# Optimization experiments

Measured on AMD Instinct MI355X. Metric: run time of the kernel, lower is better.

Reference implementation:

```python
import jax, jax.numpy as jnp
import numpy as np

D_MODEL = 512; D_STATE = 64; D_CONV = 4; HEADDIM = 64
D_INNER = 2 * D_MODEL              # expand=2
NHEADS = D_INNER // HEADDIM        # 16
CONV_DIM = D_INNER + 2 * D_STATE   # 1152
D_IN_PROJ = 2 * D_INNER + 2 * D_STATE + NHEADS  # 2192
BATCH, SEQ = 4, 1024
EPS = 1e-5


def rmsnorm(x, w):
    return x * jax.lax.rsqrt(jnp.mean(x * x, axis=-1, keepdims=True) + EPS) * w


def mamba2(u, in_w, conv_w, conv_b, dt_bias, A_log, D, gnorm_w, out_w):
    b, l, _ = u.shape
    zxbcdt = u @ in_w.T                                  # [b,l,D_IN_PROJ]
    z = zxbcdt[..., :D_INNER]
    xBC = zxbcdt[..., D_INNER:D_INNER + CONV_DIM]
    dt = jax.nn.softplus(zxbcdt[..., -NHEADS:] + dt_bias)  # [b,l,h]
    # causal depthwise conv1d (kernel D_CONV, left pad) + silu
    pad = jnp.pad(xBC, ((0, 0), (D_CONV - 1, 0), (0, 0)))
    acc = conv_b
    for k in range(D_CONV):
        acc = acc + pad[:, k:k + l, :] * conv_w[:, k]
    xBC = jax.nn.silu(acc)
    x = xBC[..., :D_INNER].reshape(b, l, NHEADS, HEADDIM)
    Bm = xBC[..., D_INNER:D_INNER + D_STATE]             # [b,l,n]
    Cm = xBC[..., D_INNER + D_STATE:]                    # [b,l,n]
    A = -jnp.exp(A_log)                                  # [h]
    decay = jnp.exp(dt * A)                              # [b,l,h]
    dtx = dt[..., None] * x                              # [b,l,h,p]

    def step(h, inp):
        dec, dx, Bt, Ct = inp
        h = h * dec[:, :, None, None] + dx[..., None] * Bt[:, None, None, :]
        y = jnp.einsum('bhpn,bn->bhp', h, Ct)
        return h, y

    h0 = jnp.zeros((b, NHEADS, HEADDIM, D_STATE), u.dtype)
    _, ys = jax.lax.scan(step, h0, (decay.transpose(1, 0, 2),
                                    dtx.transpose(1, 0, 2, 3),
                                    Bm.transpose(1, 0, 2),
                                    Cm.transpose(1, 0, 2)))
    y = ys.transpose(1, 0, 2, 3) + x * D[None, None, :, None]  # [b,l,h,p]
    y = y.reshape(b, l, D_INNER)
    y = rmsnorm(y * jax.nn.silu(z), gnorm_w)             # gated RMSNorm
    return y @ out_w.T


def setup_inputs() -> dict:
    key = jax.random.key(0)
    ks = iter(jax.random.split(key, 32))
    def rn(shape, scale=0.02):
        return jax.random.normal(next(ks), shape, dtype=jnp.float32) * scale
    inp = {
        'x': jax.random.normal(next(ks), (BATCH, SEQ, D_MODEL), dtype=jnp.float32),
        'norm_w': jnp.ones((D_MODEL,), jnp.float32),
    }
    for p in ('f', 'b'):
        inp[p + '_in_w'] = rn((D_IN_PROJ, D_MODEL))
        inp[p + '_conv_w'] = rn((CONV_DIM, D_CONV), 0.1)
        inp[p + '_conv_b'] = jnp.zeros((CONV_DIM,), jnp.float32)
        inp[p + '_dt_bias'] = rn((NHEADS,), 0.5)
        inp[p + '_A_log'] = jnp.log(jnp.arange(1, NHEADS + 1, dtype=jnp.float32))
        inp[p + '_D'] = jnp.ones((NHEADS,), jnp.float32)
        inp[p + '_gnorm_w'] = jnp.ones((D_INNER,), jnp.float32)
        inp[p + '_out_w'] = rn((D_MODEL, D_INNER))
    inp['proj_w'] = rn((D_MODEL, 2 * D_MODEL))
    return inp


def reference(x, norm_w,
              f_in_w, f_conv_w, f_conv_b, f_dt_bias, f_A_log, f_D, f_gnorm_w, f_out_w,
              b_in_w, b_conv_w, b_conv_b, b_dt_bias, b_A_log, b_D, b_gnorm_w, b_out_w,
              proj_w):
    h = rmsnorm(x, norm_w)
    fo = mamba2(h, f_in_w, f_conv_w, f_conv_b, f_dt_bias, f_A_log, f_D, f_gnorm_w, f_out_w)
    bo = jnp.flip(mamba2(jnp.flip(h, 1), b_in_w, b_conv_w, b_conv_b, b_dt_bias,
                         b_A_log, b_D, b_gnorm_w, b_out_w), 1)
    return x + jnp.concatenate([fo, bo], axis=-1) @ proj_w.T
```

## Files before the change

### kernel.cpp

```cpp
#include <hip/hip_runtime.h>
#include <math.h>

typedef unsigned short u16;
typedef __bf16  bf16x8 __attribute__((ext_vector_type(8)));
typedef float   f32x4  __attribute__((ext_vector_type(4)));
typedef unsigned short u16x8 __attribute__((ext_vector_type(8)));

#define SEQ 1024
#define MR  4096
#define DIP 2192
#define DI  1024
#define NH  16
#define CD  1152
#define NCH 32
#define CT  32
#define NIN (DIP*512)
#define NOUT (512*1024)

__device__ __forceinline__ u16 f2bf(float f) {
  union { float f; unsigned u; } v; v.f = f;
  unsigned r = v.u + 0x7FFFu + ((v.u >> 16) & 1u);
  return (u16)(r >> 16);
}
__device__ __forceinline__ float bf2f(u16 h) {
  union { unsigned u; float f; } v; v.u = ((unsigned)h) << 16; return v.f;
}
__device__ __forceinline__ void splitbf(float v, u16& h, u16& l) {
  h = f2bf(v); l = f2bf(v - bf2f(h));
}
__device__ __forceinline__ float sigm(float x){ return 1.f/(1.f+__expf(-x)); }

__device__ __forceinline__ unsigned packbf(float v) {
  u16 hh, ll; splitbf(v, hh, ll);
  return (unsigned)hh | ((unsigned)ll << 16);
}
__device__ __forceinline__ float unpackf(unsigned w) {
  return bf2f((u16)w) + bf2f((u16)(w >> 16));
}

__device__ __forceinline__ void split8(const float* p, bf16x8& H, bf16x8& L) {
  float4 a = *(const float4*)p, b = *(const float4*)(p+4);
  u16x8 hu, lu; u16 hh, ll;
  splitbf(a.x,hh,ll); hu[0]=hh; lu[0]=ll;
  splitbf(a.y,hh,ll); hu[1]=hh; lu[1]=ll;
  splitbf(a.z,hh,ll); hu[2]=hh; lu[2]=ll;
  splitbf(a.w,hh,ll); hu[3]=hh; lu[3]=ll;
  splitbf(b.x,hh,ll); hu[4]=hh; lu[4]=ll;
  splitbf(b.y,hh,ll); hu[5]=hh; lu[5]=ll;
  splitbf(b.z,hh,ll); hu[6]=hh; lu[6]=ll;
  splitbf(b.w,hh,ll); hu[7]=hh; lu[7]=ll;
  H = __builtin_bit_cast(bf16x8, hu);
  L = __builtin_bit_cast(bf16x8, lu);
}
__device__ __forceinline__ void unpack8(const unsigned* p, bf16x8& H, bf16x8& L) {
  uint4 a = *(const uint4*)p, b = *(const uint4*)(p+4);
  u16x8 hu, lu;
  hu[0]=(u16)a.x; lu[0]=(u16)(a.x>>16);
  hu[1]=(u16)a.y; lu[1]=(u16)(a.y>>16);
  hu[2]=(u16)a.z; lu[2]=(u16)(a.z>>16);
  hu[3]=(u16)a.w; lu[3]=(u16)(a.w>>16);
  hu[4]=(u16)b.x; lu[4]=(u16)(b.x>>16);
  hu[5]=(u16)b.y; lu[5]=(u16)(b.y>>16);
  hu[6]=(u16)b.z; lu[6]=(u16)(b.z>>16);
  hu[7]=(u16)b.w; lu[7]=(u16)(b.w>>16);
  H = __builtin_bit_cast(bf16x8, hu);
  L = __builtin_bit_cast(bf16x8, lu);
}
__device__ __forceinline__ void unpack8s(const unsigned* p, int stride, bf16x8& H, bf16x8& L) {
  u16x8 hu, lu;
  #pragma unroll
  for (int jj=0;jj<8;jj++){ unsigned w = p[(size_t)jj*stride]; hu[jj]=(u16)w; lu[jj]=(u16)(w>>16); }
  H = __builtin_bit_cast(bf16x8, hu);
  L = __builtin_bit_cast(bf16x8, lu);
}

__device__ __forceinline__ void gl16(const u16* g, u16* l) {
  __builtin_amdgcn_global_load_lds((const __attribute__((address_space(1))) void*)g,
                                   (__attribute__((address_space(3))) void*)l,
                                   16, 0, 0);
}

__global__ __launch_bounds__(256) void cast_all(
  const float* __restrict__ f_in, const float* __restrict__ b_in,
  const float* __restrict__ f_out, const float* __restrict__ b_out,
  const float* __restrict__ proj,
  u16* __restrict__ H, u16* __restrict__ L)
{
  int i = blockIdx.x*256 + threadIdx.x;
  constexpr int TOT = 2*NIN + 3*NOUT;
  if (i >= TOT) return;
  float v;
  if (i < NIN)               v = f_in[i];
  else if (i < 2*NIN)        v = b_in[i-NIN];
  else if (i < 2*NIN+NOUT)   v = f_out[i-2*NIN];
  else if (i < 2*NIN+2*NOUT) v = b_out[i-2*NIN-NOUT];
  else                       v = proj[i-2*NIN-2*NOUT];
  u16 hh, ll; splitbf(v, hh, ll);
  H[i] = hh; L[i] = ll;
}

__global__ __launch_bounds__(256) void rmsnorm_x(const float* __restrict__ x,
                                                 const float* __restrict__ w,
                                                 u16* __restrict__ hbh,
                                                 u16* __restrict__ hbl){
  int m = blockIdx.x, tid = threadIdx.x;
  const float* xr = x + (size_t)m*512;
  float2 v = *(const float2*)&xr[tid*2];
  float ss = v.x*v.x + v.y*v.y;
  #pragma unroll
  for (int off=32; off; off>>=1) ss += __shfl_xor(ss, off, 64);
  __shared__ float red[4];
  if ((tid&63)==0) red[tid>>6] = ss;
  __syncthreads();
  float total = red[0]+red[1]+red[2]+red[3];
  float rs = rsqrtf(total*(1.f/512.f) + 1e-5f);
  float2 w2 = *(const float2*)&w[tid*2];
  u16 h0,l0,h1,l1;
  splitbf(v.x*rs*w2.x, h0, l0);
  splitbf(v.y*rs*w2.y, h1, l1);
  *(unsigned*)&hbh[(size_t)m*512 + tid*2] = (unsigned)h0 | ((unsigned)h1<<16);
  *(unsigned*)&hbl[(size_t)m*512 + tid*2] = (unsigned)l0 | ((unsigned)l1<<16);
}

__global__ __launch_bounds__(256) void gemm_in(
    const u16* __restrict__ Ah, const u16* __restrict__ Al,
    const u16* __restrict__ Wh, const u16* __restrict__ Wl,
    float* __restrict__ C0)
{
  constexpr int K = 512;
  constexpr int N = DIP;
  __shared__ __align__(16) u16 sAh[128*32];
  __shared__ __align__(16) u16 sAl[128*32];
  __shared__ __align__(16) u16 sBh[128*32];
  __shared__ __align__(16) u16 sBl[128*32];
  const int tid = threadIdx.x;
  const int dir = blockIdx.z;
  const int m0 = blockIdx.x * 128;
  const int n0 = blockIdx.y * 128;
  const int lane = tid & 63;
  const int wid  = tid >> 6;
  const u16* wh_p = Wh + (size_t)dir*NIN;
  const u16* wl_p = Wl + (size_t)dir*NIN;
  const int j0 = wid, j1 = wid + 4;
  const int cp = lane & 3;
  auto goff = [&](int j, bool isB)->size_t {
    int row = 16*j + (lane>>2);
    int s = (row>>1) & 3;
    int kc = (cp ^ s) * 8;
    int grow;
    if (!isB) {
      grow = m0 + row;
      if (dir) grow = (grow & ~1023) + (1023 - (grow & 1023));
    } else {
      grow = n0 + row;
      if (grow >= N) grow = N-1;
    }
    return (size_t)grow*K + kc;
  };
  const size_t a0 = goff(j0,false), a1 = goff(j1,false);
  const size_t b0 = goff(j0,true),  b1 = goff(j1,true);
  const int wm = (wid & 1) * 64;
  const int wn = (wid >> 1) * 64;
  const int quad = lane >> 4;
  const int l16  = lane & 15;
  const int qx = quad ^ ((l16>>1)&3);
  const int baseA = ((wm + l16)*4 + qx)*8;
  const int baseB = ((wn + l16)*4 + qx)*8;
  f32x4 acc[4][4] = {};
  for (int kt = 0; kt < K; kt += 32) {
    __syncthreads();
    gl16(Ah + a0 + kt, &sAh[j0*512]);  gl16(Ah + a1 + kt, &sAh[j1*512]);
    gl16(Al + a0 + kt, &sAl[j0*512]);  gl16(Al + a1 + kt, &sAl[j1*512]);
    gl16(wh_p + b0 + kt, &sBh[j0*512]);  gl16(wh_p + b1 + kt, &sBh[j1*512]);
    gl16(wl_p + b0 + kt, &sBl[j0*512]);  gl16(wl_p + b1 + kt, &sBl[j1*512]);
    __syncthreads();
    bf16x8 ah[4], al[4], bh[4], bl[4];
    #pragma unroll
    for (int i=0;i<4;i++) {
      ah[i] = *(const bf16x8*)&sAh[baseA + i*512];
      al[i] = *(const bf16x8*)&sAl[baseA + i*512];
    }
    #pragma unroll
    for (int j=0;j<4;j++) {
      bh[j] = *(const bf16x8*)&sBh[baseB + j*512];
      bl[j] = *(const bf16x8*)&sBl[baseB + j*512];
    }
    #pragma unroll
    for (int i=0;i<4;i++)
      #pragma unroll
      for (int j=0;j<4;j++) {
        f32x4 t = __builtin_amdgcn_mfma_f32_16x16x32_bf16(ah[i], bl[j], acc[i][j], 0,0,0);
        t       = __builtin_amdgcn_mfma_f32_16x16x32_bf16(al[i], bh[j], t,         0,0,0);
        acc[i][j] = __builtin_amdgcn_mfma_f32_16x16x32_bf16(ah[i], bh[j], t,       0,0,0);
      }
  }
  #pragma unroll
  for (int i=0;i<4;i++)
  #pragma unroll
  for (int j=0;j<4;j++)
  #pragma unroll
  for (int r=0;r<4;r++) {
    int mo = m0 + wm + i*16 + quad*4 + r;
    int no = n0 + wn + j*16 + l16;
    if (no < N) C0[((size_t)dir*MR + mo)*DIP + no] = acc[i][j][r];
  }
}

template<int MODE>
__global__ __launch_bounds__(256) void gemm_out(
    const u16* __restrict__ Ah, const u16* __restrict__ Al,
    const u16* __restrict__ Wh, const u16* __restrict__ Wl,
    float* __restrict__ C0, const float* __restrict__ X0,
    u16* __restrict__ C1h, u16* __restrict__ C1l)
{
  constexpr int K = 1024;
  __shared__ __align__(16) u16 sAh[64*32];
  __shared__ __align__(16) u16 sAl[64*32];
  __shared__ __align__(16) u16 sBh[128*32];
  __shared__ __align__(16) u16 sBl[128*32];
  const int tid = threadIdx.x;
  const int dir = blockIdx.z;
  const int m0 = blockIdx.x * 64;
  const int n0 = blockIdx.y * 128;
  const int lane = tid & 63;
  const int wid  = tid >> 6;
  const u16* ah_p = Ah + ((MODE==1) ? (size_t)dir*MR*K : 0);
  const u16* al_p = Al + ((MODE==1) ? (size_t)dir*MR*K : 0);
  const u16* wh_p = Wh + ((MODE==1) ? (size_t)dir*NOUT : 0);
  const u16* wl_p = Wl + ((MODE==1) ? (size_t)dir*NOUT : 0);
  const int cp = lane & 3;
  auto goff = [&](int j, bool isB)->size_t {
    int row = 16*j + (lane>>2);
    int s = (row>>1) & 3;
    int kc = (cp ^ s) * 8;
    int grow = (isB ? n0 : m0) + row;
    return (size_t)grow*K + kc;
  };
  const size_t a0 = goff(wid,false);
  const size_t b0 = goff(wid,true), b1 = goff(wid+4,true);
  const int quad = lane >> 4;
  const int l16  = lane & 15;
  const int qx = quad ^ ((l16>>1)&3);
  const int baseA = (l16*4 + qx)*8;
  const int baseB = ((wid*32 + l16)*4 + qx)*8;
  f32x4 acc[4][2] = {};
  for (int kt = 0; kt < K; kt += 32) {
    __syncthreads();
    gl16(ah_p + a0 + kt, &sAh[wid*512]);
    gl16(al_p + a0 + kt, &sAl[wid*512]);
    gl16(wh_p + b0 + kt, &sBh[wid*512]);  gl16(wh_p + b1 + kt, &sBh[(wid+4)*512]);
    gl16(wl_p + b0 + kt, &sBl[wid*512]);  gl16(wl_p + b1 + kt, &sBl[(wid+4)*512]);
    __syncthreads();
    bf16x8 ah[4], al[4], bh[2], bl[2];
    #pragma unroll
    for (int i=0;i<4;i++) {
      ah[i] = *(const bf16x8*)&sAh[baseA + i*512];
      al[i] = *(const bf16x8*)&sAl[baseA + i*512];
    }
    #pragma unroll
    for (int j=0;j<2;j++) {
      bh[j] = *(const bf16x8*)&sBh[baseB + j*512];
      bl[j] = *(const bf16x8*)&sBl[baseB + j*512];
    }
    #pragma unroll
    for (int i=0;i<4;i++)
      #pragma unroll
      for (int j=0;j<2;j++) {
        f32x4 t = __builtin_amdgcn_mfma_f32_16x16x32_bf16(ah[i], bl[j], acc[i][j], 0,0,0);
        t       = __builtin_amdgcn_mfma_f32_16x16x32_bf16(al[i], bh[j], t,         0,0,0);
        acc[i][j] = __builtin_amdgcn_mfma_f32_16x16x32_bf16(ah[i], bh[j], t,       0,0,0);
      }
  }
  #pragma unroll
  for (int i=0;i<4;i++)
  #pragma unroll
  for (int j=0;j<2;j++)
  #pragma unroll
  for (int r=0;r<4;r++) {
    int mo = m0 + i*16 + quad*4 + r;
    int no = n0 + wid*32 + j*16 + l16;
    float v = acc[i][j][r];
    if (MODE==1) {
      int ro = mo;
      if (dir) ro = (mo & ~1023) + (1023 - (mo & 1023));
      u16 hh, ll; splitbf(v, hh, ll);
      C1h[(size_t)ro*DI + dir*512 + no] = hh;
      C1l[(size_t)ro*DI + dir*512 + no] = ll;
    } else {
      C0[(size_t)mo*512 + no] = v + X0[(size_t)mo*512 + no];
    }
  }
}

__global__ __launch_bounds__(320) void conv_dt(
  const float* __restrict__ Z,
  const float* __restrict__ f_cw, const float* __restrict__ f_cb,
  const float* __restrict__ b_cw, const float* __restrict__ b_cb,
  const float* __restrict__ f_dtb, const float* __restrict__ b_dtb,
  unsigned* __restrict__ xconv,
  unsigned* __restrict__ Bc, unsigned* __restrict__ Cc,
  float* __restrict__ dtq)
{
  int bm = blockIdx.x;
  int dir = bm >> 12;
  int t = bm & 1023;
  const float* cw  = dir ? b_cw : f_cw;
  const float* cb  = dir ? b_cb : f_cb;
  const float* dtb = dir ? b_dtb : f_dtb;
  int tid = threadIdx.x;
  if (tid < 288) {
    int c0 = tid*4;
    const float* zbase = Z + (size_t)(bm-3)*DIP + 1024 + c0;
    float4 w0 = *(const float4*)&cw[c0*4];
    float4 w1 = *(const float4*)&cw[(c0+1)*4];
    float4 w2 = *(const float4*)&cw[(c0+2)*4];
    float4 w3 = *(const float4*)&cw[(c0+3)*4];
    float4 z0 = {0,0,0,0}, z1 = {0,0,0,0}, z2 = {0,0,0,0};
    float4 z3 = *(const float4*)(zbase + 3*(size_t)DIP);
    if (t >= 3) {
      z0 = *(const float4*)(zbase);
      z1 = *(const float4*)(zbase + (size_t)DIP);
      z2 = *(const float4*)(zbase + 2*(size_t)DIP);
    } else {
      if (t >= 1) z2 = *(const float4*)(zbase + 2*(size_t)DIP);
      if (t >= 2) z1 = *(const float4*)(zbase + (size_t)DIP);
    }
    float4 a = *(const float4*)&cb[c0];
    a.x += z0.x*w0.x + z1.x*w0.y + z2.x*w0.z + z3.x*w0.w;
    a.y += z0.y*w1.x + z1.y*w1.y + z2.y*w1.z + z3.y*w1.w;
    a.z += z0.z*w2.x + z1.z*w2.y + z2.z*w2.z + z3.z*w2.w;
    a.w += z0.w*w3.x + z1.w*w3.y + z2.w*w3.z + z3.w*w3.w;
    float4 v;
    v.x = a.x * sigm(a.x); v.y = a.y * sigm(a.y);
    v.z = a.z * sigm(a.z); v.w = a.w * sigm(a.w);
    uint4 pv;
    pv.x = packbf(v.x); pv.y = packbf(v.y);
    pv.z = packbf(v.z); pv.w = packbf(v.w);
    if (c0 < 1024)      *(uint4*)&xconv[(size_t)bm*DI + c0] = pv;
    else if (c0 < 1088) *(uint4*)&Bc[(size_t)bm*64 + (c0-1024)] = pv;
    else                *(uint4*)&Cc[(size_t)bm*64 + (c0-1088)] = pv;
  }
  if (tid < NH) {
    float dtraw = Z[(size_t)bm*DIP + 2176 + tid] + dtb[tid];
    float dt = (dtraw > 20.f) ? dtraw : log1pf(__expf(dtraw));
    dtq[(size_t)bm*NH + tid] = dt;
  }
}

__global__ __launch_bounds__(256) void scan_mfma(
  const float* __restrict__ dtq, const unsigned* __restrict__ xconv,
  const unsigned* __restrict__ Bc, const unsigned* __restrict__ Cc,
  const float* __restrict__ f_Al, const float* __restrict__ b_Al,
  float* __restrict__ yraw, float* __restrict__ cumdec, float* __restrict__ S)
{
  __shared__ __align__(16) u16 sMh[4][32*40];
  __shared__ __align__(16) u16 sMl[4][32*40];
  __shared__ float scum[4][32];
  __shared__ float sdt[4][32];
  int bx = blockIdx.x;
  int hq = bx & 3, chunk = (bx>>2)&(NCH-1), dirb = bx>>7;
  int w = threadIdx.x >> 6, lane = threadIdx.x & 63;
  int h = hq*4 + w;
  int base_row = dirb*1024 + chunk*CT;
  const int quad = lane >> 4, l16 = lane & 15;
  const float* Al = (dirb >= 4) ? b_Al : f_Al;
  float A = -__expf(Al[h]);
  float dtl = 0.f, cum = 0.f;
  if (lane < 32) { dtl = dtq[(size_t)(base_row + lane)*16 + h]; cum = dtl; }
  #pragma unroll
  for (int off=1; off<32; off<<=1) {
    int src = (lane >= off) ? lane-off : lane;
    float o = __shfl(cum, src);
    if (lane >= off && lane < 32) cum += o;
  }
  if (lane < 32) {
    sdt[w][lane]  = dtl;
    scum[w][lane] = cum;
    cumdec[(size_t)(base_row + lane)*16 + h] = __expf(A*cum);
  }
  bf16x8 chf[2][2], clf[2][2], bhf[2][2], blf[2][2];
  #pragma unroll
  for (int i=0;i<2;i++)
  #pragma unroll
  for (int kk=0;kk<2;kk++) {
    unpack8(Cc + (size_t)(base_row + 16*i + l16)*64 + kk*32 + quad*8, chf[i][kk], clf[i][kk]);
    unpack8(Bc + (size_t)(base_row + 16*i + l16)*64 + kk*32 + quad*8, bhf[i][kk], blf[i][kk]);
  }
  f32x4 g[2][2];
  __builtin_amdgcn_s_setprio(1);
  #pragma unroll
  for (int i=0;i<2;i++)
  #pragma unroll
  for (int j=0;j<2;j++) {
    f32x4 acc = {};
    #pragma unroll
    for (int kk=0;kk<2;kk++) {
      acc = __builtin_amdgcn_mfma_f32_16x16x32_bf16(chf[i][kk], blf[j][kk], acc, 0,0,0);
      acc = __builtin_amdgcn_mfma_f32_16x16x32_bf16(clf[i][kk], bhf[j][kk], acc, 0,0,0);
      acc = __builtin_amdgcn_mfma_f32_16x16x32_bf16(chf[i][kk], bhf[j][kk], acc, 0,0,0);
    }
    g[i][j] = acc;
  }
  __builtin_amdgcn_s_setprio(0);
  float ctt[2][4];
  #pragma unroll
  for (int i=0;i<2;i++)
  #pragma unroll
  for (int r=0;r<4;r++) ctt[i][r] = scum[w][16*i + quad*4 + r];
  #pragma unroll
  for (int j=0;j<2;j++) {
    int s = 16*j + l16;
    float cts = scum[w][s];
    float dts = sdt[w][s];
    #pragma unroll
    for (int i=0;i<2;i++)
    #pragma unroll
    for (int r=0;r<4;r++) {
      int t = 16*i + quad*4 + r;
      float mv = (s <= t) ? g[i][j][r] * __expf(A*(ctt[i][r]-cts)) * dts : 0.f;
      u16 hh, ll; splitbf(mv, hh, ll);
      sMh[w][t*40 + s] = hh;
      sMl[w][t*40 + s] = ll;
    }
  }
  bf16x8 xhf[4], xlf[4];
  const unsigned* xp = xconv + (size_t)(base_row + quad*8)*1024 + h*64 + l16;
  #pragma unroll
  for (int jp=0;jp<4;jp++) unpack8s(xp + 16*jp, 1024, xhf[jp], xlf[jp]);
  bf16x8 mhf[2], mlf[2];
  #pragma unroll
  for (int i=0;i<2;i++) {
    mhf[i] = *(const bf16x8*)&sMh[w][(16*i + l16)*40 + quad*8];
    mlf[i] = *(const bf16x8*)&sMl[w][(16*i + l16)*40 + quad*8];
  }
  __builtin_amdgcn_s_setprio(1);
  #pragma unroll
  for (int i=0;i<2;i++)
  #pragma unroll
  for (int jp=0;jp<4;jp++) {
    f32x4 acc = {};
    acc = __builtin_amdgcn_mfma_f32_16x16x32_bf16(mhf[i], xlf[jp], acc, 0,0,0);
    acc = __builtin_amdgcn_mfma_f32_16x16x32_bf16(mlf[i], xhf[jp], acc, 0,0,0);
    acc = __builtin_amdgcn_mfma_f32_16x16x32_bf16(mhf[i], xhf[jp], acc, 0,0,0);
    #pragma unroll
    for (int r=0;r<4;r++)
      yraw[(size_t)(base_row + 16*i + quad*4 + r)*1024 + h*64 + 16*jp + l16] = acc[r];
  }
  __builtin_amdgcn_s_setprio(0);
  float wv[8];
  float ct31 = scum[w][31];
  #pragma unroll
  for (int jj=0;jj<8;jj++) {
    int s = quad*8 + jj;
    wv[jj] = sdt[w][s] * __expf(A*(ct31 - scum[w][s]));
  }
  bf16x8 wbh[4], wbl[4];
  #pragma unroll
  for (int j2=0;j2<4;j2++) {
    u16x8 hu, lu; u16 hh, ll;
    #pragma unroll
    for (int jj=0;jj<8;jj++) {
      float b = unpackf(Bc[(size_t)(base_row + quad*8 + jj)*64 + 16*j2 + l16]);
      splitbf(wv[jj]*b, hh, ll); hu[jj]=hh; lu[jj]=ll;
    }
    wbh[j2] = __builtin_bit_cast(bf16x8, hu);
    wbl[j2] = __builtin_bit_cast(bf16x8, lu);
  }
  size_t inst = ((size_t)(dirb*16+h)*NCH + chunk)*4096;
  __builtin_amdgcn_s_setprio(1);
  #pragma unroll
  for (int mp=0;mp<4;mp++)
  #pragma unroll
  for (int j2=0;j2<4;j2++) {
    f32x4 acc = {};
    acc = __builtin_amdgcn_mfma_f32_16x16x32_bf16(xhf[mp], wbl[j2], acc, 0,0,0);
    acc = __builtin_amdgcn_mfma_f32_16x16x32_bf16(xlf[mp], wbh[j2], acc, 0,0,0);
    acc = __builtin_amdgcn_mfma_f32_16x16x32_bf16(xhf[mp], wbh[j2], acc, 0,0,0);
    #pragma unroll
    for (int r=0;r<4;r++)
      S[inst + (size_t)(16*mp + quad*4 + r)*64 + 16*j2 + l16] = acc[r];
  }
  __builtin_amdgcn_s_setprio(0);
}

__global__ __launch_bounds__(256) void scan_comb(
  const float* __restrict__ cumdec, float* __restrict__ S)
{
  int ih = blockIdx.x >> 4;
  int sub = blockIdx.x & 15;
  int dirb = ih >> 4, h = ih & 15;
  int elem = sub*256 + threadIdx.x;
  size_t base = (size_t)ih*NCH*4096 + elem;
  float hr = 0.f;
  for (int c=0;c<NCH;c++) {
    float P = cumdec[((size_t)(dirb*1024 + c*CT + CT-1))*16 + h];
    float s = S[base + c*4096];
    S[base + c*4096] = __builtin_bit_cast(float, packbf(hr));
    hr = fmaf(hr, P, s);
  }
}

__global__ __launch_bounds__(256) void scan_y2(
  const unsigned* __restrict__ Cc, const float* __restrict__ cumdec,
  const float* __restrict__ S, float* __restrict__ yraw)
{
  int bx = blockIdx.x;
  int hq = bx & 3, chunk = (bx>>2)&(NCH-1), dirb = bx>>7;
  if (chunk == 0) return;
  int w = threadIdx.x >> 6, lane = threadIdx.x & 63;
  int h = hq*4 + w;
  int row0 = dirb*1024 + chunk*CT;
  const int quad = lane>>4, l16 = lane&15;
  size_t inst = ((size_t)(dirb*16+h)*NCH + chunk)*4096;
  float at[2][4];
  #pragma unroll
  for (int i=0;i<2;i++)
  #pragma unroll
  for (int r=0;r<4;r++)
    at[i][r] = cumdec[(size_t)(row0 + 16*i + quad*4 + r)*16 + h];
  bf16x8 chf[2][2], clf[2][2];
  #pragma unroll
  for (int i=0;i<2;i++)
  #pragma unroll
  for (int kk=0;kk<2;kk++)
    unpack8(Cc + (size_t)(row0 + 16*i + l16)*64 + kk*32 + quad*8, chf[i][kk], clf[i][kk]);
  const unsigned* Sp = (const unsigned*)S;
  bf16x8 hhf[4][2], hlf[4][2];
  #pragma unroll
  for (int j=0;j<4;j++)
  #pragma unroll
  for (int kk=0;kk<2;kk++)
    unpack8(Sp + inst + (size_t)(16*j + l16)*64 + kk*32 + quad*8, hhf[j][kk], hlf[j][kk]);
  __builtin_amdgcn_s_setprio(1);
  #pragma unroll
  for (int i=0;i<2;i++)
  #pragma unroll
  for (int j=0;j<4;j++) {
    f32x4 acc = {};
    #pragma unroll
    for (int kk=0;kk<2;kk++) {
      acc = __builtin_amdgcn_mfma_f32_16x16x32_bf16(chf[i][kk], hlf[j][kk], acc, 0,0,0);
      acc = __builtin_amdgcn_mfma_f32_16x16x32_bf16(clf[i][kk], hhf[j][kk], acc, 0,0,0);
      acc = __builtin_amdgcn_mfma_f32_16x16x32_bf16(chf[i][kk], hhf[j][kk], acc, 0,0,0);
    }
    #pragma unroll
    for (int r=0;r<4;r++) {
      size_t idx = (size_t)(row0 + 16*i + quad*4 + r)*1024 + h*64 + 16*j + l16;
      yraw[idx] += at[i][r]*acc[r];
    }
  }
  __builtin_amdgcn_s_setprio(0);
}

__global__ __launch_bounds__(256) void gate_norm(
  const float* __restrict__ yraw, const unsigned* __restrict__ xconv,
  const float* __restrict__ Z,
  const float* __restrict__ f_D, const float* __restrict__ b_D,
  const float* __restrict__ f_gw, const float* __restrict__ b_gw,
  u16* __restrict__ ygh, u16* __restrict__ ygl)
{
  int bm = blockIdx.x, tid = threadIdx.x;
  int dir = bm >> 12;
  const float* Dp = dir ? b_D : f_D;
  const float* gw = dir ? b_gw : f_gw;
  int c0 = tid*4;
  float4 y4 = *(const float4*)&yraw [(size_t)bm*DI + c0];
  uint4  xw = *(const uint4*)&xconv[(size_t)bm*DI + c0];
  float4 z4 = *(const float4*)&Z[(size_t)bm*DIP + c0];
  float Dv = Dp[c0>>6];
  float4 x4;
  x4.x = unpackf(xw.x); x4.y = unpackf(xw.y);
  x4.z = unpackf(xw.z); x4.w = unpackf(xw.w);
  float4 v;
  v.x = (y4.x + x4.x*Dv) * (z4.x * sigm(z4.x));
  v.y = (y4.y + x4.y*Dv) * (z4.y * sigm(z4.y));
  v.z = (y4.z + x4.z*Dv) * (z4.z * sigm(z4.z));
  v.w = (y4.w + x4.w*Dv) * (z4.w * sigm(z4.w));
  float ss = v.x*v.x + v.y*v.y + v.z*v.z + v.w*v.w;
  #pragma unroll
  for (int off=32; off; off>>=1) ss += __shfl_xor(ss, off, 64);
  __shared__ float red[4];
  if ((tid&63)==0) red[tid>>6] = ss;
  __syncthreads();
  float total = red[0]+red[1]+red[2]+red[3];
  float rs = rsqrtf(total*(1.f/1024.f) + 1e-5f);
  float4 g4 = *(const float4*)&gw[c0];
  ushort4 hh, ll;
  splitbf(v.x*rs*g4.x, hh.x, ll.x);
  splitbf(v.y*rs*g4.y, hh.y, ll.y);
  splitbf(v.z*rs*g4.z, hh.z, ll.z);
  splitbf(v.w*rs*g4.w, hh.w, ll.w);
  *(ushort4*)&ygh[(size_t)bm*DI + c0] = hh;
  *(ushort4*)&ygl[(size_t)bm*DI + c0] = ll;
}

extern "C" void kernel_launch(void* const* d_in, const int* in_sizes, int n_in,
                              void* d_out, int out_size, void* d_ws, size_t ws_size,
                              hipStream_t stream)
{
  const float* x        = (const float*)d_in[0];
  const float* norm_w   = (const float*)d_in[1];
  const float* f_in_w   = (const float*)d_in[2];
  const float* f_conv_w = (const float*)d_in[3];
  const float* f_conv_b = (const float*)d_in[4];
  const float* f_dt_bias= (const float*)d_in[5];
  const float* f_A_log  = (const float*)d_in[6];
  const float* f_D      = (const float*)d_in[7];
  const float* f_gw     = (const float*)d_in[8];
  const float* f_out_w  = (const float*)d_in[9];
  const float* b_in_w   = (const float*)d_in[10];
  const float* b_conv_w = (const float*)d_in[11];
  const float* b_conv_b = (const float*)d_in[12];
  const float* b_dt_bias= (const float*)d_in[13];
  const float* b_A_log  = (const float*)d_in[14];
  const float* b_D      = (const float*)d_in[15];
  const float* b_gw     = (const float*)d_in[16];
  const float* b_out_w  = (const float*)d_in[17];
  const float* proj_w   = (const float*)d_in[18];

  char* ws = (char*)d_ws;
  size_t off = 0;
  auto alloc = [&](size_t bytes)->char* {
    char* p = ws + off; off = (off + bytes + 255) & ~(size_t)255; return p;
  };
  constexpr size_t WTOT = 2*(size_t)NIN + 3*(size_t)NOUT;
  u16*   hbh   = (u16*)  alloc((size_t)MR*512*2);
  u16*   hbl   = (u16*)  alloc((size_t)MR*512*2);
  u16*   wH    = (u16*)  alloc(WTOT*2);
  u16*   wL    = (u16*)  alloc(WTOT*2);
  float* Z     = (float*)alloc(2*(size_t)MR*DIP*4);
  unsigned* xconv = (unsigned*)alloc(2*(size_t)MR*DI*4);
  unsigned* Bc    = (unsigned*)alloc(2*(size_t)MR*64*4);
  unsigned* Cc    = (unsigned*)alloc(2*(size_t)MR*64*4);
  float* dtq   = (float*)alloc(2*(size_t)MR*NH*4);
  float* cumdec= (float*)alloc(2*(size_t)MR*NH*4);
  float* S     = (float*)alloc((size_t)4096*4096*4);
  float* yraw  = (float*)alloc(2*(size_t)MR*DI*4);
  u16* wih = wH;                   u16* wil = wL;
  u16* woh = wH + 2*(size_t)NIN;   u16* wol = wL + 2*(size_t)NIN;
  u16* wph = woh + 2*(size_t)NOUT; u16* wpl = wol + 2*(size_t)NOUT;
  u16* ycath = (u16*)((char*)S);
  u16* ycatl = (u16*)((char*)S + ((size_t)MR*DI*2));
  u16* ygh   = (u16*)((char*)S + 2*((size_t)MR*DI*2));
  u16* ygl   = (u16*)((char*)S + 4*((size_t)MR*DI*2));

  cast_all<<<(int)((WTOT+255)/256),256,0,stream>>>(f_in_w, b_in_w, f_out_w, b_out_w, proj_w, wH, wL);

  rmsnorm_x<<<MR,256,0,stream>>>(x, norm_w, hbh, hbl);
  gemm_in<<<dim3(32,18,2),256,0,stream>>>(hbh, hbl, wih, wil, Z);
  conv_dt<<<2*MR,320,0,stream>>>(Z, f_conv_w, f_conv_b, b_conv_w, b_conv_b,
                                 f_dt_bias, b_dt_bias, xconv, Bc, Cc, dtq);
  scan_mfma<<<1024,256,0,stream>>>(dtq, xconv, Bc, Cc, f_A_log, b_A_log,
                                   yraw, cumdec, S);
  scan_comb<<<2048,256,0,stream>>>(cumdec, S);
  scan_y2<<<1024,256,0,stream>>>(Cc, cumdec, S, yraw);
  gate_norm<<<2*MR,256,0,stream>>>(yraw, xconv, Z, f_D, b_D, f_gw, b_gw, ygh, ygl);
  gemm_out<1><<<dim3(64,4,2),256,0,stream>>>(ygh, ygl, woh, wol, nullptr, nullptr, ycath, ycatl);
  gemm_out<2><<<dim3(64,4,1),256,0,stream>>>(ycath, ycatl, wph, wpl, (float*)d_out, x, nullptr, nullptr);
}
```

Baseline: 376.9 us.

## Fuse chunk-state output scan with gated RMSNorm and write into Z buffer

Merges the inter-chunk y correction kernel and the gated RMSNorm kernel into one 1024-thread kernel. Each block covers one 32-row chunk across all 16 heads and stages the gated values in a large LDS tile to compute the row RMS. This removes the read-modify-write of yraw between kernels and one launch. The normalized bf16 hi/lo output is written into the no-longer-needed xBC columns of Z, and the out-projection GEMM reads it there with a strided row pitch. In exchange it uses about 130KB of LDS per block, which limits occupancy to one block per CU and leaves only 256 blocks in the grid.

```diff
diff --git a/kernel.cpp b/kernel.cpp
--- a/kernel.cpp
+++ b/kernel.cpp
@@ -16,6 +16,7 @@
 #define CT  32
 #define NIN (DIP*512)
 #define NOUT (512*1024)
+#define ZROW 4384
 
 __device__ __forceinline__ u16 f2bf(float f) {
   union { float f; unsigned u; } v; v.f = f;
@@ -38,20 +39,6 @@
   return bf2f((u16)w) + bf2f((u16)(w >> 16));
 }
 
-__device__ __forceinline__ void split8(const float* p, bf16x8& H, bf16x8& L) {
-  float4 a = *(const float4*)p, b = *(const float4*)(p+4);
-  u16x8 hu, lu; u16 hh, ll;
-  splitbf(a.x,hh,ll); hu[0]=hh; lu[0]=ll;
-  splitbf(a.y,hh,ll); hu[1]=hh; lu[1]=ll;
-  splitbf(a.z,hh,ll); hu[2]=hh; lu[2]=ll;
-  splitbf(a.w,hh,ll); hu[3]=hh; lu[3]=ll;
-  splitbf(b.x,hh,ll); hu[4]=hh; lu[4]=ll;
-  splitbf(b.y,hh,ll); hu[5]=hh; lu[5]=ll;
-  splitbf(b.z,hh,ll); hu[6]=hh; lu[6]=ll;
-  splitbf(b.w,hh,ll); hu[7]=hh; lu[7]=ll;
-  H = __builtin_bit_cast(bf16x8, hu);
-  L = __builtin_bit_cast(bf16x8, lu);
-}
 __device__ __forceinline__ void unpack8(const unsigned* p, bf16x8& H, bf16x8& L) {
   uint4 a = *(const uint4*)p, b = *(const uint4*)(p+4);
   u16x8 hu, lu;
@@ -214,6 +201,7 @@
     u16* __restrict__ C1h, u16* __restrict__ C1l)
 {
   constexpr int K = 1024;
+  constexpr int AS = (MODE==1) ? ZROW : 1024;
   __shared__ __align__(16) u16 sAh[64*32];
   __shared__ __align__(16) u16 sAl[64*32];
   __shared__ __align__(16) u16 sBh[128*32];
@@ -224,8 +212,8 @@
   const int n0 = blockIdx.y * 128;
   const int lane = tid & 63;
   const int wid  = tid >> 6;
-  const u16* ah_p = Ah + ((MODE==1) ? (size_t)dir*MR*K : 0);
-  const u16* al_p = Al + ((MODE==1) ? (size_t)dir*MR*K : 0);
+  const u16* ah_p = Ah + ((MODE==1) ? (size_t)dir*MR*AS : 0);
+  const u16* al_p = Al + ((MODE==1) ? (size_t)dir*MR*AS : 0);
   const u16* wh_p = Wh + ((MODE==1) ? (size_t)dir*NOUT : 0);
   const u16* wl_p = Wl + ((MODE==1) ? (size_t)dir*NOUT : 0);
   const int cp = lane & 3;
@@ -234,7 +222,7 @@
     int s = (row>>1) & 3;
     int kc = (cp ^ s) * 8;
     int grow = (isB ? n0 : m0) + row;
-    return (size_t)grow*K + kc;
+    return (size_t)grow*(isB ? (size_t)K : (size_t)AS) + kc;
   };
   const size_t a0 = goff(wid,false);
   const size_t b0 = goff(wid,true), b1 = goff(wid+4,true);
@@ -500,98 +488,118 @@
   }
 }
 
-__global__ __launch_bounds__(256) void scan_y2(
+__global__ __launch_bounds__(1024) void scan_y2_gate(
   const unsigned* __restrict__ Cc, const float* __restrict__ cumdec,
-  const float* __restrict__ S, float* __restrict__ yraw)
-{
+  const float* __restrict__ S, const float* __restrict__ yraw,
+  const unsigned* __restrict__ xconv, const float* Z, u16* zt,
+  const float* __restrict__ f_D, const float* __restrict__ b_D,
+  const float* __restrict__ f_gw, const float* __restrict__ b_gw)
+{
+  __shared__ float vbuf[32][1028];
+  __shared__ float red[32][17];
+  __shared__ float rsb[32];
   int bx = blockIdx.x;
-  int hq = bx & 3, chunk = (bx>>2)&(NCH-1), dirb = bx>>7;
-  if (chunk == 0) return;
+  int chunk = bx & (NCH-1), dirb = bx >> 5;
   int w = threadIdx.x >> 6, lane = threadIdx.x & 63;
-  int h = hq*4 + w;
+  int h = w;
+  int dir = dirb >> 2;
   int row0 = dirb*1024 + chunk*CT;
   const int quad = lane>>4, l16 = lane&15;
-  size_t inst = ((size_t)(dirb*16+h)*NCH + chunk)*4096;
-  float at[2][4];
+  const float* Dp  = dir ? b_D  : f_D;
+  const float* gwp = dir ? b_gw : f_gw;
+  float Dv = Dp[h];
+
+  f32x4 acc[2][4] = {};
+  float at[2][4] = {};
+  if (chunk > 0) {
+    size_t inst = ((size_t)(dirb*16+h)*NCH + chunk)*4096;
+    #pragma unroll
+    for (int i=0;i<2;i++)
+    #pragma unroll
+    for (int r=0;r<4;r++)
+      at[i][r] = cumdec[(size_t)(row0 + 16*i + quad*4 + r)*16 + h];
+    bf16x8 chf[2][2], clf[2][2];
+    #pragma unroll
+    for (int i=0;i<2;i++)
+    #pragma unroll
+    for (int kk=0;kk<2;kk++)
+      unpack8(Cc + (size_t)(row0 + 16*i + l16)*64 + kk*32 + quad*8, chf[i][kk], clf[i][kk]);
+    const unsigned* Sp = (const unsigned*)S;
+    __builtin_amdgcn_s_setprio(1);
+    #pragma unroll
+    for (int j=0;j<4;j++) {
+      bf16x8 hhf[2], hlf[2];
+      #pragma unroll
+      for (int kk=0;kk<2;kk++)
+        unpack8(Sp + inst + (size_t)(16*j + l16)*64 + kk*32 + quad*8, hhf[kk], hlf[kk]);
+      #pragma unroll
+      for (int i=0;i<2;i++) {
+        f32x4 a2 = acc[i][j];
+        #pragma unroll
+        for (int kk=0;kk<2;kk++) {
+          a2 = __builtin_amdgcn_mfma_f32_16x16x32_bf16(chf[i][kk], hlf[kk], a2, 0,0,0);
+          a2 = __builtin_amdgcn_mfma_f32_16x16x32_bf16(clf[i][kk], hhf[kk], a2, 0,0,0);
+          a2 = __builtin_amdgcn_mfma_f32_16x16x32_bf16(chf[i][kk], hhf[kk], a2, 0,0,0);
+        }
+        acc[i][j] = a2;
+      }
+    }
+    __builtin_amdgcn_s_setprio(0);
+  }
+  float pss[2][4] = {};
   #pragma unroll
   for (int i=0;i<2;i++)
   #pragma unroll
-  for (int r=0;r<4;r++)
-    at[i][r] = cumdec[(size_t)(row0 + 16*i + quad*4 + r)*16 + h];
-  bf16x8 chf[2][2], clf[2][2];
+  for (int r=0;r<4;r++) {
+    int t = 16*i + quad*4 + r;
+    size_t g = (size_t)(row0 + t);
+    #pragma unroll
+    for (int j=0;j<4;j++) {
+      int c = h*64 + 16*j + l16;
+      float yv = yraw[g*1024 + c];
+      float xv = unpackf(xconv[g*1024 + c]);
+      float zv = Z[g*DIP + c];
+      float v = (yv + xv*Dv + at[i][r]*acc[i][j][r]) * (zv * sigm(zv));
+      vbuf[t][c] = v;
+      pss[i][r] += v*v;
+    }
+  }
   #pragma unroll
   for (int i=0;i<2;i++)
   #pragma unroll
-  for (int kk=0;kk<2;kk++)
-    unpack8(Cc + (size_t)(row0 + 16*i + l16)*64 + kk*32 + quad*8, chf[i][kk], clf[i][kk]);
-  const unsigned* Sp = (const unsigned*)S;
-  bf16x8 hhf[4][2], hlf[4][2];
-  #pragma unroll
-  for (int j=0;j<4;j++)
-  #pragma unroll
-  for (int kk=0;kk<2;kk++)
-    unpack8(Sp + inst + (size_t)(16*j + l16)*64 + kk*32 + quad*8, hhf[j][kk], hlf[j][kk]);
-  __builtin_amdgcn_s_setprio(1);
+  for (int r=0;r<4;r++) {
+    float s2 = pss[i][r];
+    s2 += __shfl_xor(s2, 1, 64);
+    s2 += __shfl_xor(s2, 2, 64);
+    s2 += __shfl_xor(s2, 4, 64);
+    s2 += __shfl_xor(s2, 8, 64);
+    if (l16 == 0) red[16*i + quad*4 + r][w] = s2;
+  }
+  __syncthreads();
+  if (threadIdx.x < 32) {
+    int t = threadIdx.x;
+    float tot = 0.f;
+    #pragma unroll
+    for (int ww=0; ww<16; ww++) tot += red[t][ww];
+    rsb[t] = rsqrtf(tot*(1.f/1024.f) + 1e-5f);
+  }
+  __syncthreads();
   #pragma unroll
   for (int i=0;i<2;i++)
   #pragma unroll
-  for (int j=0;j<4;j++) {
-    f32x4 acc = {};
-    #pragma unroll
-    for (int kk=0;kk<2;kk++) {
-      acc = __builtin_amdgcn_mfma_f32_16x16x32_bf16(chf[i][kk], hlf[j][kk], acc, 0,0,0);
-      acc = __builtin_amdgcn_mfma_f32_16x16x32_bf16(clf[i][kk], hhf[j][kk], acc, 0,0,0);
-      acc = __builtin_amdgcn_mfma_f32_16x16x32_bf16(chf[i][kk], hhf[j][kk], acc, 0,0,0);
-    }
-    #pragma unroll
-    for (int r=0;r<4;r++) {
-      size_t idx = (size_t)(row0 + 16*i + quad*4 + r)*1024 + h*64 + 16*j + l16;
-      yraw[idx] += at[i][r]*acc[r];
-    }
-  }
-  __builtin_amdgcn_s_setprio(0);
-}
-
-__global__ __launch_bounds__(256) void gate_norm(
-  const float* __restrict__ yraw, const unsigned* __restrict__ xconv,
-  const float* __restrict__ Z,
-  const float* __restrict__ f_D, const float* __restrict__ b_D,
-  const float* __restrict__ f_gw, const float* __restrict__ b_gw,
-  u16* __restrict__ ygh, u16* __restrict__ ygl)
-{
-  int bm = blockIdx.x, tid = threadIdx.x;
-  int dir = bm >> 12;
-  const float* Dp = dir ? b_D : f_D;
-  const float* gw = dir ? b_gw : f_gw;
-  int c0 = tid*4;
-  float4 y4 = *(const float4*)&yraw [(size_t)bm*DI + c0];
-  uint4  xw = *(const uint4*)&xconv[(size_t)bm*DI + c0];
-  float4 z4 = *(const float4*)&Z[(size_t)bm*DIP + c0];
-  float Dv = Dp[c0>>6];
-  float4 x4;
-  x4.x = unpackf(xw.x); x4.y = unpackf(xw.y);
-  x4.z = unpackf(xw.z); x4.w = unpackf(xw.w);
-  float4 v;
-  v.x = (y4.x + x4.x*Dv) * (z4.x * sigm(z4.x));
-  v.y = (y4.y + x4.y*Dv) * (z4.y * sigm(z4.y));
-  v.z = (y4.z + x4.z*Dv) * (z4.z * sigm(z4.z));
-  v.w = (y4.w + x4.w*Dv) * (z4.w * sigm(z4.w));
-  float ss = v.x*v.x + v.y*v.y + v.z*v.z + v.w*v.w;
-  #pragma unroll
-  for (int off=32; off; off>>=1) ss += __shfl_xor(ss, off, 64);
-  __shared__ float red[4];
-  if ((tid&63)==0) red[tid>>6] = ss;
-  __syncthreads();
-  float total = red[0]+red[1]+red[2]+red[3];
-  float rs = rsqrtf(total*(1.f/1024.f) + 1e-5f);
-  float4 g4 = *(const float4*)&gw[c0];
-  ushort4 hh, ll;
-  splitbf(v.x*rs*g4.x, hh.x, ll.x);
-  splitbf(v.y*rs*g4.y, hh.y, ll.y);
-  splitbf(v.z*rs*g4.z, hh.z, ll.z);
-  splitbf(v.w*rs*g4.w, hh.w, ll.w);
-  *(ushort4*)&ygh[(size_t)bm*DI + c0] = hh;
-  *(ushort4*)&ygl[(size_t)bm*DI + c0] = ll;
+  for (int r=0;r<4;r++) {
+    int t = 16*i + quad*4 + r;
+    size_t g = (size_t)(row0 + t);
+    float rs = rsb[t];
+    #pragma unroll
+    for (int j=0;j<4;j++) {
+      int c = h*64 + 16*j + l16;
+      float o = vbuf[t][c] * rs * gwp[c];
+      u16 hh, ll; splitbf(o, hh, ll);
+      zt[g*ZROW + 2048 + c] = hh;
+      zt[g*ZROW + 3072 + c] = ll;
+    }
+  }
 }
 
 extern "C" void kernel_launch(void* const* d_in, const int* in_sizes, int n_in,
@@ -641,8 +649,6 @@
   u16* wph = woh + 2*(size_t)NOUT; u16* wpl = wol + 2*(size_t)NOUT;
   u16* ycath = (u16*)((char*)S);
   u16* ycatl = (u16*)((char*)S + ((size_t)MR*DI*2));
-  u16* ygh   = (u16*)((char*)S + 2*((size_t)MR*DI*2));
-  u16* ygl   = (u16*)((char*)S + 4*((size_t)MR*DI*2));
 
   cast_all<<<(int)((WTOT+255)/256),256,0,stream>>>(f_in_w, b_in_w, f_out_w, b_out_w, proj_w, wH, wL);
 
@@ -653,8 +659,10 @@
   scan_mfma<<<1024,256,0,stream>>>(dtq, xconv, Bc, Cc, f_A_log, b_A_log,
                                    yraw, cumdec, S);
   scan_comb<<<2048,256,0,stream>>>(cumdec, S);
-  scan_y2<<<1024,256,0,stream>>>(Cc, cumdec, S, yraw);
-  gate_norm<<<2*MR,256,0,stream>>>(yraw, xconv, Z, f_D, b_D, f_gw, b_gw, ygh, ygl);
-  gemm_out<1><<<dim3(64,4,2),256,0,stream>>>(ygh, ygl, woh, wol, nullptr, nullptr, ycath, ycatl);
-  gemm_out<2><<<dim3(64,4,1),256,0,stream>>>(ycath, ycatl, wph, wpl, (float*)d_out, x, nullptr, nullptr);
-}
+  scan_y2_gate<<<256,1024,0,stream>>>(Cc, cumdec, S, yraw, xconv, Z, (u16*)Z,
+                                      f_D, b_D, f_gw, b_gw);
+  gemm_out<1><<<dim3(64,4,2),256,0,stream>>>((u16*)Z + 2048, (u16*)Z + 3072,
+                                             woh, wol, nullptr, nullptr, ycath, ycatl);
+  gemm_out<2><<<dim3(64,4,1),256,0,stream>>>(ycath, ycatl, wph, wpl,
+                                             (float*)d_out, x, nullptr, nullptr);
+}
```

Measured after the change: 368.1 us. 1.02x faster.
